# Kernel optimization log

Measured on AMD Instinct MI355X. Metric: run time of the kernel, lower is better.

## Reference

```python
import jax, jax.numpy as jnp
import numpy as np

N = 50000   # num nodes
D = 64      # feature dim
E = 800000  # num edges (avg degree 16)


def setup_inputs() -> dict:
    key = jax.random.key(0)
    k1, k2, k3 = jax.random.split(key, 3)
    x = jax.random.normal(k1, (N, D), dtype=jnp.float32)
    edge_index = jax.random.randint(k2, (2, E), 0, N, dtype=jnp.int32)
    edge_weight = jax.random.uniform(k3, (E,), dtype=jnp.float32)
    return {"x": x, "edge_index": edge_index, "edge_weight": edge_weight}


def reference(x, edge_index, edge_weight):
    """Faithful translation of scatter_median (spmm with reduce='median'):
    per destination node, the (lower) median over its weighted incoming
    neighbor messages, computed independently per feature channel.
    Nodes with zero in-degree produce zeros (as in the torch code where
    h is initialized to zeros and degree-0 rows are skipped).
    """
    n, d = x.shape
    e = edge_index.shape[1]

    # sort edges by destination (stable sort; within-segment order is irrelevant for median)
    order = jnp.argsort(edge_index[1])
    row = edge_index[0, order]
    col = edge_index[1, order]
    w = edge_weight[order]

    # weighted messages: x_j = x[row] * w  -> [E, D]
    x_j = x[row] * w[:, None]

    # per-destination degree and position of each edge within its segment
    deg = jnp.bincount(col, length=n)                                   # [N]
    starts = jnp.concatenate([jnp.zeros(1, deg.dtype), jnp.cumsum(deg)[:-1]])
    pos = jnp.arange(e, dtype=deg.dtype) - starts[col]                  # [E]

    # dense batch [N, max_deg, D], padded with +inf so pads sort to the end
    max_deg = int(jnp.max(deg))  # concrete on materialized inputs
    dense = jnp.full((n, max_deg, d), jnp.inf, dtype=x.dtype)
    dense = dense.at[col, pos].set(x_j)

    # per-channel sort, then pick the lower-median index (torch.median semantics:
    # for even counts it returns the lower of the two middle values)
    dense = jnp.sort(dense, axis=1)
    idx = jnp.maximum((deg - 1) // 2, 0)                                # [N]
    med = jnp.take_along_axis(dense, idx[:, None, None], axis=1)[:, 0]  # [N, D]

    return jnp.where(deg[:, None] > 0, med, jnp.zeros((), dtype=x.dtype))
```

## Files before the change

kernel.cpp:

```cpp
#include <hip/hip_runtime.h>
#include <stdint.h>
#include <math.h>

#define NN 50000
#define DD 64
#define EE 800000
#define BSZ 64
#define NB 782
#define BCAP 1280
#define EPW 4096
#define CAP 48
#define BIGMAX 1024


__global__ void zero_cnt(int* __restrict__ cnt) {
    int i = blockIdx.x * blockDim.x + threadIdx.x;
    if (i < NB + 1) cnt[i] = 0;
}

__global__ __launch_bounds__(512) void bucketize(
        const int* __restrict__ ei, const float* __restrict__ ew,
        int* __restrict__ bucket_cnt, uint64_t* __restrict__ recs) {
    __shared__ int   hist[NB];
    __shared__ int   base[NB];
    __shared__ int   eL[EPW];
    __shared__ int   dL[EPW];
    __shared__ float wL[EPW];
    const int t = threadIdx.x;
    const int e0 = blockIdx.x * EPW;
    const int nE = (e0 + EPW < EE) ? EPW : (EE - e0);

    for (int i = t; i < NB; i += 512) hist[i] = 0;
    for (int i = t; i < nE; i += 512) {
        eL[i] = ei[e0 + i];
        dL[i] = ei[EE + e0 + i];
        wL[i] = ew[e0 + i];
    }
    __syncthreads();

    for (int i = t; i < nE; i += 512)
        atomicAdd(&hist[dL[i] >> 6], 1);
    __syncthreads();

    for (int i = t; i < NB; i += 512) {
        int c = hist[i];
        base[i] = (c > 0) ? atomicAdd(&bucket_cnt[i], c) : 0;
        hist[i] = 0;
    }
    __syncthreads();

    for (int i = t; i < nE; i += 512) {
        int d = dL[i];
        int b = d >> 6;
        int p = base[b] + atomicAdd(&hist[b], 1);
        if (p < BCAP)
            recs[(size_t)b * BCAP + p] =
                ((uint64_t)__float_as_uint(wL[i]) << 32) |
                ((uint32_t)eL[i] << 6) | (uint32_t)(d & 63);
    }
}

__global__ __launch_bounds__(256) void bin_dense(
        const int* __restrict__ bucket_cnt, const uint64_t* __restrict__ recs,
        uint64_t* __restrict__ slots, int* __restrict__ deg,
        int* __restrict__ big_cnt, int* __restrict__ big_list) {
    __shared__ uint64_t sl[BSZ * CAP];
    __shared__ int degl[BSZ];
    const int t = threadIdx.x;
    const int b = blockIdx.x;

    int cnt = bucket_cnt[b];
    if (cnt > BCAP) cnt = BCAP;

    for (int i = t; i < BSZ; i += 256) degl[i] = 0;
    __syncthreads();

    const uint64_t* br = recs + (size_t)b * BCAP;
    for (int i = t; i < cnt; i += 256) {
        uint64_t r = br[i];
        int loc = (int)(r & 63u);
        int p = atomicAdd(&degl[loc], 1);
        if (p < CAP)
            sl[loc * CAP + p] = (r & 0xFFFFFFFF00000000ull)
                              | (uint32_t)(((uint32_t)r) >> 6);
    }
    __syncthreads();

    uint64_t* outrow = slots + (size_t)b * BSZ * CAP;
    for (int i = t; i < BSZ * CAP; i += 256) outrow[i] = sl[i];
    int n0 = b * BSZ;
    for (int i = t; i < BSZ; i += 256) {
        int n = n0 + i;
        if (n < NN) {
            int dgi = degl[i];
            if (dgi > CAP) dgi = CAP;
            deg[n] = dgi;
            if (dgi > 32) {
                int q = atomicAdd(big_cnt, 1);
                if (q < BIGMAX) big_list[q] = n;
            }
        }
    }
}

__device__ __forceinline__ void cswap(float& a, float& b) {
    float lo = fminf(a, b);
    float hi = fmaxf(a, b);
    a = lo; b = hi;
}

template<int I, int END, int R, int STEP, int AW>
struct Pairs {
    static __device__ __forceinline__ void run(float (&r)[AW]) {
        if constexpr (I + R < END) {
            cswap(r[I], r[I + R]);
            Pairs<I + STEP, END, R, STEP, AW>::run(r);
        }
    }
};

template<int LO, int N, int R, int AW>
struct Merge {
    static __device__ __forceinline__ void run(float (&r)[AW]) {
        if constexpr (2 * R < N) {
            Merge<LO,     N, 2 * R, AW>::run(r);
            Merge<LO + R, N, 2 * R, AW>::run(r);
            Pairs<LO + R, LO + N, R, 2 * R, AW>::run(r);
        } else {
            cswap(r[LO], r[LO + R]);
        }
    }
};

template<int LO, int N, int AW>
struct Sorter {
    static __device__ __forceinline__ void run(float (&r)[AW]) {
        if constexpr (N > 1) {
            Sorter<LO,         N / 2, AW>::run(r);
            Sorter<LO + N / 2, N / 2, AW>::run(r);
            Merge<LO, N, 1, AW>::run(r);
        }
    }
};

template <int PW>
__device__ __forceinline__ float gather_sort_u(const float* __restrict__ x, int lane,
                                               int dg, int k,
                                               const uint64_t* __restrict__ row) {
    float r[PW];
    #pragma unroll
    for (int j = 0; j < PW; ++j) {
        float v = INFINITY;
        if (j < dg) {
            uint64_t s = row[j];
            uint32_t src = (uint32_t)(s & 0xffffffffu);
            float    w   = __uint_as_float((uint32_t)(s >> 32));
            v = x[(size_t)src * DD + lane] * w;
        }
        r[j] = v;
    }
    Sorter<0, PW, PW>::run(r);
    constexpr int KLO = PW / 4;
    constexpr int KHI = (PW / 2 > 0) ? PW / 2 - 1 : 0;
    float med = r[KLO];
    #pragma unroll
    for (int t = KLO + 1; t <= KHI; ++t)
        if (t == k) med = r[t];
    return med;
}

__global__ __launch_bounds__(256, 4) void median_main(
    const float* __restrict__ x, const int* __restrict__ deg,
    const uint64_t* __restrict__ slots, float* __restrict__ out) {
    const int lane = threadIdx.x & 63;
    const int wid  = (blockIdx.x * blockDim.x + threadIdx.x) >> 6;
    const int S    = (gridDim.x * blockDim.x) >> 6;

    for (int n0 = wid; n0 < NN; n0 += S) {
        const int n = __builtin_amdgcn_readfirstlane(n0);
        int dg = __builtin_amdgcn_readfirstlane(deg[n]);
        if (dg > 32) continue;

        float med = 0.f;
        if (dg > 0) {
            const uint64_t* row = slots + (size_t)n * CAP;
            const int k = (dg - 1) >> 1;
            if      (dg <= 2)  med = gather_sort_u<2>(x, lane, dg, k, row);
            else if (dg <= 4)  med = gather_sort_u<4>(x, lane, dg, k, row);
            else if (dg <= 8)  med = gather_sort_u<8>(x, lane, dg, k, row);
            else if (dg <= 16) med = gather_sort_u<16>(x, lane, dg, k, row);
            else               med = gather_sort_u<32>(x, lane, dg, k, row);
        }
        out[(size_t)n * DD + lane] = med;
    }
}

__global__ __launch_bounds__(256) void median_big(
    const float* __restrict__ x, const int* __restrict__ deg,
    const uint64_t* __restrict__ slots, const int* __restrict__ big_cnt,
    const int* __restrict__ big_list, float* __restrict__ out) {
    const int lane = threadIdx.x & 63;
    const int wid  = (blockIdx.x * blockDim.x + threadIdx.x) >> 6;
    const int S    = (gridDim.x * blockDim.x) >> 6;

    int cnt = __builtin_amdgcn_readfirstlane(big_cnt[0]);
    if (cnt > BIGMAX) cnt = BIGMAX;

    for (int i = wid; i < cnt; i += S) {
        int n  = __builtin_amdgcn_readfirstlane(big_list[i]);
        int dg = __builtin_amdgcn_readfirstlane(deg[n]);
        const uint64_t* row = slots + (size_t)n * CAP;
        float r[64];
        #pragma unroll
        for (int j = 0; j < 64; ++j) {
            float v = INFINITY;
            if (j < dg) {
                uint64_t s = row[j];
                uint32_t src = (uint32_t)(s & 0xffffffffu);
                float    w   = __uint_as_float((uint32_t)(s >> 32));
                v = x[(size_t)src * DD + lane] * w;
            }
            r[j] = v;
        }
        Sorter<0, 64, 64>::run(r);
        const int k = (dg - 1) >> 1;
        float med = r[16];
        #pragma unroll
        for (int t = 17; t <= 31; ++t)
            if (t == k) med = r[t];
        out[(size_t)n * DD + lane] = med;
    }
}

extern "C" void kernel_launch(void* const* d_in, const int* in_sizes, int n_in,
                              void* d_out, int out_size, void* d_ws, size_t ws_size,
                              hipStream_t stream) {
    const float*  x  = (const float*)d_in[0];
    const int*    ei = (const int*)d_in[1];
    const float*  ew = (const float*)d_in[2];
    float* out = (float*)d_out;

    int*      bucket_cnt = (int*)d_ws;
    int*      big_cnt    = bucket_cnt + NB;
    int*      big_list   = (int*)((char*)d_ws + (1 << 12));
    int*      deg        = (int*)((char*)d_ws + (1 << 14));
    uint64_t* recs       = (uint64_t*)((char*)d_ws + (1 << 18));
    uint64_t* slots      = (uint64_t*)((char*)d_ws + (1 << 23));

    zero_cnt<<<(NB + 1 + 255) / 256, 256, 0, stream>>>(bucket_cnt);
    bucketize<<<(EE + EPW - 1) / EPW, 512, 0, stream>>>(ei, ew, bucket_cnt, recs);
    bin_dense<<<NB, 256, 0, stream>>>(bucket_cnt, recs, slots, deg, big_cnt, big_list);
    median_main<<<2048, 256, 0, stream>>>(x, deg, slots, out);
    median_big<<<16, 256, 0, stream>>>(x, deg, slots, big_cnt, big_list, out);
}
```

Measured before the change: 142.4 us.

## Locally sort edges by bucket in LDS before coalesced record writes

The bucketize kernel now counts edges per destination bucket, runs an in-block prefix scan, and places the packed records in shared memory sorted by bucket. A second pass then writes each bucket's records to global memory as contiguous runs, replacing the previous scattered 8-byte stores. The per-block edge chunk is doubled, which halves the number of global atomics on bucket counters but costs more LDS and fewer blocks. The edge arrays are now read from global memory twice instead of once.

```diff
diff --git a/kernel.cpp b/kernel.cpp
--- a/kernel.cpp
+++ b/kernel.cpp
@@ -7,8 +7,9 @@
 #define EE 800000
 #define BSZ 64
 #define NB 782
+#define NBP 1024
 #define BCAP 1280
-#define EPW 4096
+#define EPW 8192
 #define CAP 48
 #define BIGMAX 1024
 
@@ -21,42 +22,67 @@
 __global__ __launch_bounds__(512) void bucketize(
         const int* __restrict__ ei, const float* __restrict__ ew,
         int* __restrict__ bucket_cnt, uint64_t* __restrict__ recs) {
-    __shared__ int   hist[NB];
-    __shared__ int   base[NB];
-    __shared__ int   eL[EPW];
-    __shared__ int   dL[EPW];
-    __shared__ float wL[EPW];
-    const int t = threadIdx.x;
+    __shared__ uint64_t       srt[EPW];
+    __shared__ unsigned short bktS[EPW];
+    __shared__ int hist[NB];
+    __shared__ int off[NBP];
+    __shared__ int base[NB];
+    const int t  = threadIdx.x;
     const int e0 = blockIdx.x * EPW;
     const int nE = (e0 + EPW < EE) ? EPW : (EE - e0);
 
     for (int i = t; i < NB; i += 512) hist[i] = 0;
-    for (int i = t; i < nE; i += 512) {
-        eL[i] = ei[e0 + i];
-        dL[i] = ei[EE + e0 + i];
-        wL[i] = ew[e0 + i];
-    }
     __syncthreads();
 
     for (int i = t; i < nE; i += 512)
-        atomicAdd(&hist[dL[i] >> 6], 1);
-    __syncthreads();
-
+        atomicAdd(&hist[ei[EE + e0 + i] >> 6], 1);
+    __syncthreads();
+
+    off[t]       = (t < NB)       ? hist[t]       : 0;
+    off[t + 512] = (t + 512 < NB) ? hist[t + 512] : 0;
+    __syncthreads();
+    for (int d = 1; d < NBP; d <<= 1) {
+        int v0 = (t       >= d) ? off[t       - d] : 0;
+        int v1 = (t + 512 >= d) ? off[t + 512 - d] : 0;
+        __syncthreads();
+        off[t]       += v0;
+        off[t + 512] += v1;
+        __syncthreads();
+    }
+    {
+        int a0 = (t < NB)       ? off[t]       - hist[t]       : 0;
+        int a1 = (t + 512 < NB) ? off[t + 512] - hist[t + 512] : 0;
+        __syncthreads();
+        off[t] = a0;
+        off[t + 512] = a1;
+    }
     for (int i = t; i < NB; i += 512) {
         int c = hist[i];
         base[i] = (c > 0) ? atomicAdd(&bucket_cnt[i], c) : 0;
-        hist[i] = 0;
-    }
+    }
+    __syncthreads();
+    for (int i = t; i < NB; i += 512) hist[i] = 0;
     __syncthreads();
 
     for (int i = t; i < nE; i += 512) {
-        int d = dL[i];
-        int b = d >> 6;
-        int p = base[b] + atomicAdd(&hist[b], 1);
-        if (p < BCAP)
-            recs[(size_t)b * BCAP + p] =
-                ((uint64_t)__float_as_uint(wL[i]) << 32) |
-                ((uint32_t)eL[i] << 6) | (uint32_t)(d & 63);
+        int   s = ei[e0 + i];
+        int   d = ei[EE + e0 + i];
+        float w = ew[e0 + i];
+        int   b = d >> 6;
+        int   p = atomicAdd(&hist[b], 1);
+        int idx = off[b] + p;
+        srt[idx]  = ((uint64_t)__float_as_uint(w) << 32) |
+                    ((uint32_t)s << 6) | (uint32_t)(d & 63);
+        bktS[idx] = (unsigned short)b;
+    }
+    __syncthreads();
+
+    for (int i = t; i < nE; i += 512) {
+        uint64_t r = srt[i];
+        int b   = bktS[i];
+        int pos = base[b] + (i - off[b]);
+        if (pos < BCAP)
+            recs[(size_t)b * BCAP + pos] = r;
     }
 }
 
```

New measurement: 150.4 us. 1.06x slower.

## Sort integer keys instead of floats and specialize degree buckets

Applied to the files above, without the earlier changes.

Maps float messages to order-preserving signed integer keys so compare-swaps use integer min/max rather than fminf/fmaxf, which may carry NaN handling overhead. Adds finer degree buckets (12, 20, 24) whose padded slots are compile-time constants, so the compiler can fold away compare-swaps against known maximum keys, and narrows the median index selection range per bucket. Also vectorizes the shared-to-global slot copy into 16-byte stores. The cost is more template instantiations and a larger code size, and NaN ordering changes.

```diff
diff --git a/kernel.cpp b/kernel.cpp
--- a/kernel.cpp
+++ b/kernel.cpp
@@ -64,7 +64,7 @@
         const int* __restrict__ bucket_cnt, const uint64_t* __restrict__ recs,
         uint64_t* __restrict__ slots, int* __restrict__ deg,
         int* __restrict__ big_cnt, int* __restrict__ big_list) {
-    __shared__ uint64_t sl[BSZ * CAP];
+    __shared__ __align__(16) uint64_t sl[BSZ * CAP];
     __shared__ int degl[BSZ];
     const int t = threadIdx.x;
     const int b = blockIdx.x;
@@ -86,8 +86,9 @@
     }
     __syncthreads();
 
-    uint64_t* outrow = slots + (size_t)b * BSZ * CAP;
-    for (int i = t; i < BSZ * CAP; i += 256) outrow[i] = sl[i];
+    ulonglong2*       o2 = (ulonglong2*)(slots + (size_t)b * BSZ * CAP);
+    const ulonglong2* s2 = (const ulonglong2*)sl;
+    for (int i = t; i < BSZ * CAP / 2; i += 256) o2[i] = s2[i];
     int n0 = b * BSZ;
     for (int i = t; i < BSZ; i += 256) {
         int n = n0 + i;
@@ -103,15 +104,15 @@
     }
 }
 
-__device__ __forceinline__ void cswap(float& a, float& b) {
-    float lo = fminf(a, b);
-    float hi = fmaxf(a, b);
+__device__ __forceinline__ void cswap(int& a, int& b) {
+    int lo = min(a, b);
+    int hi = max(a, b);
     a = lo; b = hi;
 }
 
 template<int I, int END, int R, int STEP, int AW>
 struct Pairs {
-    static __device__ __forceinline__ void run(float (&r)[AW]) {
+    static __device__ __forceinline__ void run(int (&r)[AW]) {
         if constexpr (I + R < END) {
             cswap(r[I], r[I + R]);
             Pairs<I + STEP, END, R, STEP, AW>::run(r);
@@ -121,7 +122,7 @@
 
 template<int LO, int N, int R, int AW>
 struct Merge {
-    static __device__ __forceinline__ void run(float (&r)[AW]) {
+    static __device__ __forceinline__ void run(int (&r)[AW]) {
         if constexpr (2 * R < N) {
             Merge<LO,     N, 2 * R, AW>::run(r);
             Merge<LO + R, N, 2 * R, AW>::run(r);
@@ -134,7 +135,7 @@
 
 template<int LO, int N, int AW>
 struct Sorter {
-    static __device__ __forceinline__ void run(float (&r)[AW]) {
+    static __device__ __forceinline__ void run(int (&r)[AW]) {
         if constexpr (N > 1) {
             Sorter<LO,         N / 2, AW>::run(r);
             Sorter<LO + N / 2, N / 2, AW>::run(r);
@@ -143,30 +144,42 @@
     }
 };
 
-template <int PW>
+__device__ __forceinline__ int f2key(float f) {
+    int s = __float_as_int(f);
+    return s ^ ((s >> 31) & 0x7fffffff);
+}
+__device__ __forceinline__ float key2f(int kk) {
+    return __int_as_float(kk ^ ((kk >> 31) & 0x7fffffff));
+}
+
+template <int PW, int REAL, int KLO, int KHI>
 __device__ __forceinline__ float gather_sort_u(const float* __restrict__ x, int lane,
                                                int dg, int k,
                                                const uint64_t* __restrict__ row) {
-    float r[PW];
+    int r[PW];
     #pragma unroll
     for (int j = 0; j < PW; ++j) {
-        float v = INFINITY;
-        if (j < dg) {
-            uint64_t s = row[j];
-            uint32_t src = (uint32_t)(s & 0xffffffffu);
-            float    w   = __uint_as_float((uint32_t)(s >> 32));
-            v = x[(size_t)src * DD + lane] * w;
-        }
-        r[j] = v;
+        int kj;
+        if (j < REAL) {
+            float v = INFINITY;
+            if (j < dg) {
+                uint64_t s = row[j];
+                uint32_t src = (uint32_t)(s & 0xffffffffu);
+                float    w   = __uint_as_float((uint32_t)(s >> 32));
+                v = x[(size_t)src * DD + lane] * w;
+            }
+            kj = f2key(v);
+        } else {
+            kj = 0x7fffffff;
+        }
+        r[j] = kj;
     }
     Sorter<0, PW, PW>::run(r);
-    constexpr int KLO = PW / 4;
-    constexpr int KHI = (PW / 2 > 0) ? PW / 2 - 1 : 0;
-    float med = r[KLO];
+    int med = r[KLO];
     #pragma unroll
     for (int t = KLO + 1; t <= KHI; ++t)
         if (t == k) med = r[t];
-    return med;
+    return key2f(med);
 }
 
 __global__ __launch_bounds__(256, 4) void median_main(
@@ -185,11 +198,14 @@
         if (dg > 0) {
             const uint64_t* row = slots + (size_t)n * CAP;
             const int k = (dg - 1) >> 1;
-            if      (dg <= 2)  med = gather_sort_u<2>(x, lane, dg, k, row);
-            else if (dg <= 4)  med = gather_sort_u<4>(x, lane, dg, k, row);
-            else if (dg <= 8)  med = gather_sort_u<8>(x, lane, dg, k, row);
-            else if (dg <= 16) med = gather_sort_u<16>(x, lane, dg, k, row);
-            else               med = gather_sort_u<32>(x, lane, dg, k, row);
+            if      (dg <= 2)  med = gather_sort_u< 2,  2,  0,  0>(x, lane, dg, k, row);
+            else if (dg <= 4)  med = gather_sort_u< 4,  4,  1,  1>(x, lane, dg, k, row);
+            else if (dg <= 8)  med = gather_sort_u< 8,  8,  2,  3>(x, lane, dg, k, row);
+            else if (dg <= 12) med = gather_sort_u<16, 12,  4,  5>(x, lane, dg, k, row);
+            else if (dg <= 16) med = gather_sort_u<16, 16,  6,  7>(x, lane, dg, k, row);
+            else if (dg <= 20) med = gather_sort_u<32, 20,  8,  9>(x, lane, dg, k, row);
+            else if (dg <= 24) med = gather_sort_u<32, 24, 10, 11>(x, lane, dg, k, row);
+            else               med = gather_sort_u<32, 32, 12, 15>(x, lane, dg, k, row);
         }
         out[(size_t)n * DD + lane] = med;
     }
@@ -210,25 +226,31 @@
         int n  = __builtin_amdgcn_readfirstlane(big_list[i]);
         int dg = __builtin_amdgcn_readfirstlane(deg[n]);
         const uint64_t* row = slots + (size_t)n * CAP;
-        float r[64];
+        int r[64];
         #pragma unroll
         for (int j = 0; j < 64; ++j) {
-            float v = INFINITY;
-            if (j < dg) {
-                uint64_t s = row[j];
-                uint32_t src = (uint32_t)(s & 0xffffffffu);
-                float    w   = __uint_as_float((uint32_t)(s >> 32));
-                v = x[(size_t)src * DD + lane] * w;
+            int kj;
+            if (j < CAP) {
+                float v = INFINITY;
+                if (j < dg) {
+                    uint64_t s = row[j];
+                    uint32_t src = (uint32_t)(s & 0xffffffffu);
+                    float    w   = __uint_as_float((uint32_t)(s >> 32));
+                    v = x[(size_t)src * DD + lane] * w;
+                }
+                kj = f2key(v);
+            } else {
+                kj = 0x7fffffff;
             }
-            r[j] = v;
+            r[j] = kj;
         }
         Sorter<0, 64, 64>::run(r);
         const int k = (dg - 1) >> 1;
-        float med = r[16];
+        int med = r[16];
         #pragma unroll
-        for (int t = 17; t <= 31; ++t)
+        for (int t = 17; t <= 23; ++t)
             if (t == k) med = r[t];
-        out[(size_t)n * DD + lane] = med;
+        out[(size_t)n * DD + lane] = key2f(med);
     }
 }
 
```

After: 132.0 us. 1.08x faster.
